# Optimization experiments

Hardware: AMD Instinct MI355X
Metric: run time of the kernel (lower is better)

## Reference

```python
import jax, jax.numpy as jnp
import numpy as np

N, E, NODE_DIM, HID = 10000, 160000, 16, 128
N_CONV = 8  # 4 encoder + 4 decoder EdgeConv layers


def setup_inputs() -> dict:
    key = jax.random.key(0)
    ks = jax.random.split(key, 12)

    def lin(k, fan_in, shape):
        return (jax.random.normal(k, shape, jnp.float32) / np.sqrt(fan_in)).astype(jnp.float32)

    return {
        "x": jax.random.normal(ks[0], (N, NODE_DIM), jnp.float32),
        "edge_index": jax.random.randint(ks[1], (2, E), 0, N, jnp.int32),
        "t": jax.random.uniform(ks[2], (1,), jnp.float32),
        "node_emb_W": lin(ks[3], NODE_DIM, (NODE_DIM, HID)),
        "node_emb_b": jnp.zeros((HID,), jnp.float32),
        "conv_W1": lin(ks[4], 2 * HID, (N_CONV, 2 * HID, HID)),
        "conv_b1": jnp.zeros((N_CONV, HID), jnp.float32),
        "conv_W2": lin(ks[5], HID, (N_CONV, HID, HID)),
        "conv_b2": jnp.zeros((N_CONV, HID), jnp.float32),
        "enc_fc_W": lin(ks[6], HID, (HID, HID)),
        "enc_fc_b": jnp.zeros((HID,), jnp.float32),
        "dec_fc_W": lin(ks[7], HID, (HID, NODE_DIM)),
        "dec_fc_b": jnp.zeros((NODE_DIM,), jnp.float32),
        "time_proj_W": lin(ks[8], 64, (64, NODE_DIM)),
        "time_proj_b": jnp.zeros((NODE_DIM,), jnp.float32),
    }


def _edge_conv(x, src, dst, W1, b1, W2, b2):
    # PyG EdgeConv (aggr='max'): message = mlp(cat[x_i, x_j - x_i]); x_i = x[dst], x_j = x[src]
    xi = x[dst]                      # [E', H]
    xj = x[src]                      # [E', H]
    m = jnp.concatenate([xi, xj - xi], axis=1)           # [E', 2H]
    m = jnp.maximum(m @ W1 + b1, 0.0) @ W2 + b2          # [E', H]
    return jax.ops.segment_max(m, dst, num_segments=x.shape[0])


def reference(x, edge_index, t, node_emb_W, node_emb_b, conv_W1, conv_b1,
              conv_W2, conv_b2, enc_fc_W, enc_fc_b, dec_fc_W, dec_fc_b,
              time_proj_W, time_proj_b):
    n = x.shape[0]
    # add_self_loops (done once; identical across layers)
    loop = jnp.arange(n, dtype=edge_index.dtype)
    src = jnp.concatenate([edge_index[0], loop])
    dst = jnp.concatenate([edge_index[1], loop])

    # sinusoidal time embedding -> projection to node_dim
    freq = jnp.exp(jnp.linspace(-4.0, 4.0, 32).astype(x.dtype))
    t_emb = jnp.concatenate([jnp.sin(t * freq), jnp.cos(t * freq)], axis=-1)  # [64]
    t_emb = t_emb @ time_proj_W + time_proj_b                                  # [node_dim]

    h = x + t_emb[None, :]
    # encoder
    h = h @ node_emb_W + node_emb_b
    for i in range(4):
        h = _edge_conv(h, src, dst, conv_W1[i], conv_b1[i], conv_W2[i], conv_b2[i])
    h = h @ enc_fc_W + enc_fc_b
    # decoder
    for i in range(4, 8):
        h = _edge_conv(h, src, dst, conv_W1[i], conv_b1[i], conv_W2[i], conv_b2[i])
    return h @ dec_fc_W + dec_fc_b
```

## Files before the change

### kernel.cpp

```cpp
#include <hip/hip_runtime.h>
#include <hip/hip_fp16.h>

typedef _Float16 half8 __attribute__((ext_vector_type(8)));
typedef float f32x4 __attribute__((ext_vector_type(4)));
typedef float f32x16 __attribute__((ext_vector_type(16)));

#define HID 128
#define NDIM 16
#define NCONV 8
#define ECAP 64

static __device__ __forceinline__ half8 load_h8(const _Float16* p) {
    return *(const half8*)p;
}

__global__ void prep_weights(const float* __restrict__ W1, const float* __restrict__ W2,
                             const float* __restrict__ dW, const float* __restrict__ b1,
                             const float* __restrict__ eW, const int* __restrict__ ei,
                             _Float16* __restrict__ WABT, _Float16* __restrict__ W2T,
                             _Float16* __restrict__ dWT, float* __restrict__ biasAB,
                             _Float16* __restrict__ eW16,
                             int* __restrict__ cnt, int* __restrict__ eltab, int E) {
    int idx = blockIdx.x * blockDim.x + threadIdx.x;
    int total = NCONV * HID * HID;
    if (idx < total) {
        int l = idx / (HID * HID);
        int r = idx % (HID * HID);
        int k = r / HID;
        int j = r % HID;
        const float* w1 = W1 + (size_t)l * 2 * HID * HID;
        float top = w1[k * HID + j];
        float bot = w1[(HID + k) * HID + j];
        _Float16* wab = WABT + (size_t)l * 2 * HID * HID;
        wab[j * HID + k] = (_Float16)(top - bot);
        wab[(HID + j) * HID + k] = (_Float16)bot;
        const float* w2 = W2 + (size_t)l * HID * HID;
        W2T[(size_t)l * HID * HID + j * HID + k] = (_Float16)w2[k * HID + j];
    } else if (idx < total + 16 * HID) {
        int r = idx - total;
        int j = r / HID;
        int k = r % HID;
        dWT[j * HID + k] = (_Float16)dW[k * NDIM + j];
    } else if (idx < total + 16 * HID + NCONV * 256) {
        int r = idx - total - 16 * HID;
        int l = r >> 8;
        int c = r & 255;
        biasAB[l * 256 + c] = (c < HID) ? b1[l * HID + c] : 0.f;
    } else if (idx < total + 16 * HID + NCONV * 256 + HID * HID) {
        int r = idx - total - 16 * HID - NCONV * 256;
        eW16[r] = (_Float16)eW[r];
    }
    int gsz = gridDim.x * blockDim.x;
    for (int e = idx; e < E; e += gsz) {
        int dv = ei[E + e];
        int pos = atomicAdd(&cnt[dv], 1);
        if (pos < ECAP) eltab[(size_t)dv * ECAP + pos] = ei[e];
    }
}

__global__ __launch_bounds__(512) void node_emb_ab(const float* __restrict__ x,
                                                   const float* __restrict__ t,
                                                   const float* __restrict__ tpW,
                                                   const float* __restrict__ tpb,
                                                   const float* __restrict__ neW,
                                                   const float* __restrict__ neb,
                                                   const _Float16* __restrict__ WABT0,
                                                   const float* __restrict__ biasAB0,
                                                   _Float16* __restrict__ Atab,
                                                   _Float16* __restrict__ Btab,
                                                   const _Float16* __restrict__ eW16,
                                                   const _Float16* __restrict__ WABT4old,
                                                   const float* __restrict__ b1_4,
                                                   const float* __restrict__ eb,
                                                   _Float16* __restrict__ WENC,
                                                   float* __restrict__ biasENC, int n) {
    int bid = blockIdx.x;
    int tid = threadIdx.x;
    int ngroups = (n + 15) >> 4;
    int lane = tid & 63;
    int wv = tid >> 6;
    int c = lane & 15;
    int kq = lane >> 4;

    if (bid >= ngroups) {
        int xb = bid - ngroups;
        if (xb < 16) {
            int gw = xb * 8 + wv;
            int jt = gw >> 3;
            int kt = gw & 7;
            half8 a[4], b[4];
            #pragma unroll
            for (int kb = 0; kb < 4; kb++) {
                a[kb] = load_h8(eW16 + (size_t)(kt * 16 + c) * HID + kb * 32 + kq * 8);
                b[kb] = load_h8(WABT4old + (size_t)(jt * 16 + c) * HID + kb * 32 + kq * 8);
            }
            f32x4 acc = {0.f, 0.f, 0.f, 0.f};
            #pragma unroll
            for (int kb = 0; kb < 4; kb++)
                acc = __builtin_amdgcn_mfma_f32_16x16x32_f16(a[kb], b[kb], acc, 0, 0, 0);
            #pragma unroll
            for (int r = 0; r < 4; r++)
                WENC[(size_t)(jt * 16 + c) * HID + kt * 16 + kq * 4 + r] = (_Float16)acc[r];
        } else if (tid < 256) {
            float acc = (tid < HID) ? b1_4[tid] : 0.f;
            const _Float16* row = WABT4old + (size_t)tid * HID;
            for (int q = 0; q < HID; q++) acc += eb[q] * (float)row[q];
            biasENC[tid] = acc;
        }
        return;
    }

    __shared__ float sc[64];
    __shared__ float temb[NDIM];
    __shared__ _Float16 hlds[16][136];
    float tv = t[0];
    if (tid < 32) {
        float f = expf(-4.0f + 8.0f * (float)tid / 31.0f);
        sc[tid] = sinf(tv * f);
        sc[32 + tid] = cosf(tv * f);
    }
    __syncthreads();
    if (tid < 16) {
        float acc = tpb[tid];
        for (int k = 0; k < 64; k++) acc += sc[k] * tpW[k * NDIM + tid];
        temb[tid] = acc;
    }
    __syncthreads();

    int gbase = bid * 16;
    for (int idx = tid; idx < 16 * HID; idx += 512) {
        int r = idx >> 7;
        int j = idx & 127;
        int v = gbase + r;
        float acc = 0.f;
        if (v < n) {
            const float* xr = x + (size_t)v * NDIM;
            acc = neb[j];
            #pragma unroll
            for (int d = 0; d < NDIM; d++) acc += (xr[d] + temb[d]) * neW[d * HID + j];
        }
        hlds[r][j] = (_Float16)acc;
    }
    __syncthreads();

    half8 a[4];
    #pragma unroll
    for (int kb = 0; kb < 4; kb++)
        a[kb] = load_h8(&hlds[c][kb * 32 + kq * 8]);
    #pragma unroll
    for (int p = 0; p < 2; p++) {
        int jt = wv + p * 8;
        int wrow = jt * 16 + c;
        f32x4 acc = {0.f, 0.f, 0.f, 0.f};
        #pragma unroll
        for (int kb = 0; kb < 4; kb++) {
            half8 b = load_h8(WABT0 + (size_t)wrow * HID + kb * 32 + kq * 8);
            acc = __builtin_amdgcn_mfma_f32_16x16x32_f16(a[kb], b, acc, 0, 0, 0);
        }
        float bv = biasAB0[wrow];
        _Float16* dst = (wrow < HID) ? Atab : Btab;
        int dcol = wrow & (HID - 1);
        #pragma unroll
        for (int r = 0; r < 4; r++) {
            int row = gbase + kq * 4 + r;
            if (row < n) dst[(size_t)row * HID + dcol] = (_Float16)(acc[r] + bv);
        }
    }
}

__global__ __launch_bounds__(512) void fused_conv(const _Float16* __restrict__ Acur,
                                                  const _Float16* __restrict__ Bcur,
                                                  const _Float16* __restrict__ W2T_l,
                                                  const float* __restrict__ b2_l,
                                                  const int* __restrict__ cnt,
                                                  const int* __restrict__ eltab,
                                                  const _Float16* __restrict__ WABT_n,
                                                  const float* __restrict__ biasAB_n,
                                                  _Float16* __restrict__ Anxt,
                                                  _Float16* __restrict__ Bnxt,
                                                  const _Float16* __restrict__ dWT,
                                                  const float* __restrict__ db,
                                                  float* __restrict__ out,
                                                  int last, int n) {
    __shared__ _Float16 w2s[2048 * 8];
    __shared__ float b2s[HID];
    __shared__ _Float16 hlds[16][136];

    int tid = threadIdx.x;
    #pragma unroll
    for (int i = 0; i < 4; i++) {
        int fid = i * 512 + tid;
        int ln = fid & 63;
        int grp = fid >> 6;
        int kb = grp >> 2;
        int cb = grp & 3;
        *(half8*)(w2s + (size_t)fid * 8) =
            load_h8(W2T_l + (size_t)(cb * 32 + (ln & 31)) * HID + kb * 16 + (ln >> 5) * 8);
    }
    if (tid < HID) b2s[tid] = b2_l[tid];
    __syncthreads();

    int lane = tid & 63;
    int wv = tid >> 6;
    int er = lane & 31;
    int hi = lane >> 5;
    int c = lane & 15;
    int kq = lane >> 4;

    int g = blockIdx.x;
    int gbase = g * 16;

    int vA = gbase + wv;
    int vB = gbase + wv + 8;
    int dgA = 0, dgB = 0;
    if (vA < n) { dgA = cnt[vA]; dgA = (dgA > ECAP) ? ECAP : dgA; }
    if (vB < n) { dgB = cnt[vB]; dgB = (dgB > ECAP) ? ECAP : dgB; }
    int srcA = (er < dgA) ? eltab[(size_t)vA * ECAP + er] : vA;
    int srcB = (er < dgB) ? eltab[(size_t)vB * ECAP + er] : vB;

    auto ec_node = [&](int v, int dg, int src0, int row) {
        float macc0 = -3.0e38f, macc1 = -3.0e38f, macc2 = -3.0e38f, macc3 = -3.0e38f;
        if (v < n) {
            int ntile = (dg + 32) >> 5;
            int src = src0;
            for (int tI = 0; tI < ntile; tI++) {
                const _Float16* ap = Acur + (size_t)v * HID + hi * 8;
                const _Float16* bp = Bcur + (size_t)src * HID + hi * 8;
                half8 s[8];
                #pragma unroll
                for (int kb = 0; kb < 8; kb++) {
                    half8 t2 = load_h8(ap + kb * 16) + load_h8(bp + kb * 16);
                    #pragma unroll
                    for (int e2 = 0; e2 < 8; e2++) t2[e2] = (t2[e2] > (_Float16)0) ? t2[e2] : (_Float16)0;
                    s[kb] = t2;
                }
                int en = (tI + 1) * 32 + er;
                int srcn = (tI + 1 < ntile && en < dg) ? eltab[(size_t)v * ECAP + en] : v;

#define CB_BLOCK(CB, MREF)                                                              \
                {                                                                       \
                    f32x16 d;                                                           \
                    _Pragma("unroll")                                                   \
                    for (int e2 = 0; e2 < 16; e2++) d[e2] = 0.f;                        \
                    _Pragma("unroll")                                                   \
                    for (int kb = 0; kb < 8; kb++) {                                    \
                        half8 w = *(const half8*)(w2s + ((size_t)((kb * 4 + CB) * 64 + lane)) * 8); \
                        d = __builtin_amdgcn_mfma_f32_32x32x16_f16(s[kb], w, d, 0, 0, 0); \
                    }                                                                   \
                    float m0 = fmaxf(fmaxf(d[0], d[1]), fmaxf(d[2], d[3]));             \
                    float m1 = fmaxf(fmaxf(d[4], d[5]), fmaxf(d[6], d[7]));             \
                    float m2 = fmaxf(fmaxf(d[8], d[9]), fmaxf(d[10], d[11]));           \
                    float m3 = fmaxf(fmaxf(d[12], d[13]), fmaxf(d[14], d[15]));         \
                    MREF = fmaxf(MREF, fmaxf(fmaxf(m0, m1), fmaxf(m2, m3)));            \
                }
                CB_BLOCK(0, macc0)
                __builtin_amdgcn_sched_barrier(0);
                CB_BLOCK(1, macc1)
                __builtin_amdgcn_sched_barrier(0);
                CB_BLOCK(2, macc2)
                __builtin_amdgcn_sched_barrier(0);
                CB_BLOCK(3, macc3)
#undef CB_BLOCK
                src = srcn;
            }
        }
        float m0 = fmaxf(macc0, __shfl_xor(macc0, 32)) + b2s[er];
        float m1 = fmaxf(macc1, __shfl_xor(macc1, 32)) + b2s[32 + er];
        float m2 = fmaxf(macc2, __shfl_xor(macc2, 32)) + b2s[64 + er];
        float m3 = fmaxf(macc3, __shfl_xor(macc3, 32)) + b2s[96 + er];
        if (lane < 32) {
            hlds[row][er]      = (_Float16)m0;
            hlds[row][32 + er] = (_Float16)m1;
            hlds[row][64 + er] = (_Float16)m2;
            hlds[row][96 + er] = (_Float16)m3;
        }
    };

    ec_node(vA, dgA, srcA, wv);
    ec_node(vB, dgB, srcB, wv + 8);
    __syncthreads();

    if (!last) {
        half8 a[4];
        #pragma unroll
        for (int kb = 0; kb < 4; kb++)
            a[kb] = load_h8(&hlds[c][kb * 32 + kq * 8]);
        #pragma unroll
        for (int p = 0; p < 2; p++) {
            int jt = wv + p * 8;
            int wrow = jt * 16 + c;
            f32x4 acc = {0.f, 0.f, 0.f, 0.f};
            #pragma unroll
            for (int kb = 0; kb < 4; kb++) {
                half8 b = load_h8(WABT_n + (size_t)wrow * HID + kb * 32 + kq * 8);
                acc = __builtin_amdgcn_mfma_f32_16x16x32_f16(a[kb], b, acc, 0, 0, 0);
            }
            float bv = biasAB_n[wrow];
            _Float16* dst = (wrow < HID) ? Anxt : Bnxt;
            int dcol = wrow & (HID - 1);
            #pragma unroll
            for (int r = 0; r < 4; r++) {
                int row = gbase + kq * 4 + r;
                if (row < n) dst[(size_t)row * HID + dcol] = (_Float16)(acc[r] + bv);
            }
        }
    } else if (wv == 0) {
        half8 a[4];
        #pragma unroll
        for (int kb = 0; kb < 4; kb++)
            a[kb] = load_h8(&hlds[c][kb * 32 + kq * 8]);
        f32x4 acc = {0.f, 0.f, 0.f, 0.f};
        #pragma unroll
        for (int kb = 0; kb < 4; kb++) {
            half8 b = load_h8(dWT + (size_t)c * HID + kb * 32 + kq * 8);
            acc = __builtin_amdgcn_mfma_f32_16x16x32_f16(a[kb], b, acc, 0, 0, 0);
        }
        float bv = db[c];
        #pragma unroll
        for (int r = 0; r < 4; r++) {
            int row = gbase + kq * 4 + r;
            if (row < n) out[(size_t)row * NDIM + c] = acc[r] + bv;
        }
    }
}

extern "C" void kernel_launch(void* const* d_in, const int* in_sizes, int n_in,
                              void* d_out, int out_size, void* d_ws, size_t ws_size,
                              hipStream_t stream) {
    const float* x   = (const float*)d_in[0];
    const int*   ei  = (const int*)d_in[1];
    const float* t   = (const float*)d_in[2];
    const float* neW = (const float*)d_in[3];
    const float* neb = (const float*)d_in[4];
    const float* cW1 = (const float*)d_in[5];
    const float* cb1 = (const float*)d_in[6];
    const float* cW2 = (const float*)d_in[7];
    const float* cb2 = (const float*)d_in[8];
    const float* eW  = (const float*)d_in[9];
    const float* eb  = (const float*)d_in[10];
    const float* dW  = (const float*)d_in[11];
    const float* db  = (const float*)d_in[12];
    const float* tpW = (const float*)d_in[13];
    const float* tpb = (const float*)d_in[14];

    int N = in_sizes[0] / NDIM;
    int E = in_sizes[1] / 2;

    char* w = (char*)d_ws;
    auto alloc = [&](size_t bytes) {
        void* p = (void*)w;
        w += (bytes + 255) & ~(size_t)255;
        return p;
    };
    _Float16*  Atab0  = (_Float16*)alloc((size_t)N * HID * 2);
    _Float16*  Btab0  = (_Float16*)alloc((size_t)N * HID * 2);
    _Float16*  Atab1  = (_Float16*)alloc((size_t)N * HID * 2);
    _Float16*  Btab1  = (_Float16*)alloc((size_t)N * HID * 2);
    _Float16*  WABT   = (_Float16*)alloc((size_t)NCONV * 2 * HID * HID * 2);
    _Float16*  W2T    = (_Float16*)alloc((size_t)NCONV * HID * HID * 2);
    _Float16*  dWT    = (_Float16*)alloc((size_t)16 * HID * 2);
    _Float16*  eW16   = (_Float16*)alloc((size_t)HID * HID * 2);
    _Float16*  WENC   = (_Float16*)alloc((size_t)2 * HID * HID * 2);
    float*     biasAB = (float*)alloc((size_t)NCONV * 256 * 4);
    float*     biasENC= (float*)alloc((size_t)256 * 4);
    int*       cnt    = (int*)alloc((size_t)N * 4);
    int*       eltab  = (int*)alloc((size_t)N * ECAP * 4);

    hipMemsetAsync(cnt, 0, (size_t)N * 4, stream);
    int prep_total = NCONV * HID * HID + 16 * HID + NCONV * 256 + HID * HID;
    prep_weights<<<(prep_total + 255) / 256, 256, 0, stream>>>(cW1, cW2, dW, cb1, eW, ei,
                                                               WABT, W2T, dWT, biasAB,
                                                               eW16, cnt, eltab, E);
    int nmt = (N + 15) / 16;
    node_emb_ab<<<nmt + 17, 512, 0, stream>>>(x, t, tpW, tpb, neW, neb,
                                              WABT, biasAB, Atab0, Btab0,
                                              eW16, WABT + (size_t)4 * 2 * HID * HID,
                                              cb1 + (size_t)4 * HID, eb, WENC, biasENC, N);

    for (int l = 0; l < NCONV; l++) {
        const _Float16* Acur = (l & 1) ? Atab1 : Atab0;
        const _Float16* Bcur = (l & 1) ? Btab1 : Btab0;
        _Float16* Anxt = (l & 1) ? Atab0 : Atab1;
        _Float16* Bnxt = (l & 1) ? Btab0 : Btab1;
        int ln = (l + 1 < NCONV) ? (l + 1) : 0;
        const _Float16* wabn = (l == 3) ? WENC : WABT + (size_t)ln * 2 * HID * HID;
        const float*    babn = (l == 3) ? biasENC : biasAB + (size_t)ln * 256;
        fused_conv<<<nmt, 512, 0, stream>>>(Acur, Bcur,
                                            W2T + (size_t)l * HID * HID,
                                            cb2 + (size_t)l * HID,
                                            cnt, eltab,
                                            wabn, babn,
                                            Anxt, Bnxt,
                                            dWT, db, (float*)d_out,
                                            (l == NCONV - 1) ? 1 : 0, N);
    }
}
```

Baseline: 253.8 us.

## Pack two low-degree nodes per MFMA tile and move edge bucketing into embed kernel

When both nodes a wave handles have at most 15 incoming edges (plus self loop), their edges are packed into one 32-row MFMA tile, so the wave runs one set of W2 MFMAs instead of two, each of which was mostly padding. Average degree is about 17 with self loops, so many node pairs qualify. The memset of the degree counters is folded into prep_weights, and the edge bucketing (atomics) moves from prep_weights into node_emb_ab, removing a memset launch. The cost is a divergent code path and more branching per block.

```diff
diff --git a/kernel.cpp b/kernel.cpp
--- a/kernel.cpp
+++ b/kernel.cpp
@@ -16,11 +16,11 @@
 
 __global__ void prep_weights(const float* __restrict__ W1, const float* __restrict__ W2,
                              const float* __restrict__ dW, const float* __restrict__ b1,
-                             const float* __restrict__ eW, const int* __restrict__ ei,
+                             const float* __restrict__ eW,
                              _Float16* __restrict__ WABT, _Float16* __restrict__ W2T,
                              _Float16* __restrict__ dWT, float* __restrict__ biasAB,
                              _Float16* __restrict__ eW16,
-                             int* __restrict__ cnt, int* __restrict__ eltab, int E) {
+                             int* __restrict__ cnt, int n) {
     int idx = blockIdx.x * blockDim.x + threadIdx.x;
     int total = NCONV * HID * HID;
     if (idx < total) {
@@ -49,12 +49,8 @@
     } else if (idx < total + 16 * HID + NCONV * 256 + HID * HID) {
         int r = idx - total - 16 * HID - NCONV * 256;
         eW16[r] = (_Float16)eW[r];
-    }
-    int gsz = gridDim.x * blockDim.x;
-    for (int e = idx; e < E; e += gsz) {
-        int dv = ei[E + e];
-        int pos = atomicAdd(&cnt[dv], 1);
-        if (pos < ECAP) eltab[(size_t)dv * ECAP + pos] = ei[e];
+    } else if (idx < total + 16 * HID + NCONV * 256 + HID * HID + n) {
+        cnt[idx - total - 16 * HID - NCONV * 256 - HID * HID] = 0;
     }
 }
 
@@ -73,9 +69,24 @@
                                                    const float* __restrict__ b1_4,
                                                    const float* __restrict__ eb,
                                                    _Float16* __restrict__ WENC,
-                                                   float* __restrict__ biasENC, int n) {
+                                                   float* __restrict__ biasENC,
+                                                   const int* __restrict__ ei,
+                                                   int* __restrict__ cnt,
+                                                   int* __restrict__ eltab,
+                                                   int n, int E) {
     int bid = blockIdx.x;
     int tid = threadIdx.x;
+
+    {
+        int gtid = bid * 512 + tid;
+        int gsz = gridDim.x * 512;
+        for (int e = gtid; e < E; e += gsz) {
+            int dv = ei[E + e];
+            int pos = atomicAdd(&cnt[dv], 1);
+            if (pos < ECAP) eltab[(size_t)dv * ECAP + pos] = ei[e];
+        }
+    }
+
     int ngroups = (n + 15) >> 4;
     int lane = tid & 63;
     int wv = tid >> 6;
@@ -215,69 +226,119 @@
     int dgA = 0, dgB = 0;
     if (vA < n) { dgA = cnt[vA]; dgA = (dgA > ECAP) ? ECAP : dgA; }
     if (vB < n) { dgB = cnt[vB]; dgB = (dgB > ECAP) ? ECAP : dgB; }
-    int srcA = (er < dgA) ? eltab[(size_t)vA * ECAP + er] : vA;
-    int srcB = (er < dgB) ? eltab[(size_t)vB * ECAP + er] : vB;
-
-    auto ec_node = [&](int v, int dg, int src0, int row) {
-        float macc0 = -3.0e38f, macc1 = -3.0e38f, macc2 = -3.0e38f, macc3 = -3.0e38f;
-        if (v < n) {
-            int ntile = (dg + 32) >> 5;
-            int src = src0;
-            for (int tI = 0; tI < ntile; tI++) {
-                const _Float16* ap = Acur + (size_t)v * HID + hi * 8;
-                const _Float16* bp = Bcur + (size_t)src * HID + hi * 8;
-                half8 s[8];
-                #pragma unroll
-                for (int kb = 0; kb < 8; kb++) {
-                    half8 t2 = load_h8(ap + kb * 16) + load_h8(bp + kb * 16);
+
+    auto write_row = [&](int row, float m0, float m1, float m2, float m3) {
+        float a0 = fmaxf(m0, __shfl_xor(m0, 32)) + b2s[er];
+        float a1 = fmaxf(m1, __shfl_xor(m1, 32)) + b2s[32 + er];
+        float a2 = fmaxf(m2, __shfl_xor(m2, 32)) + b2s[64 + er];
+        float a3 = fmaxf(m3, __shfl_xor(m3, 32)) + b2s[96 + er];
+        if (lane < 32) {
+            hlds[row][er]      = (_Float16)a0;
+            hlds[row][32 + er] = (_Float16)a1;
+            hlds[row][64 + er] = (_Float16)a2;
+            hlds[row][96 + er] = (_Float16)a3;
+        }
+    };
+
+    bool packed = (vB < n) && (dgA <= 15) && (dgB <= 15);
+    if (packed) {
+        int pnode = (er < 16) ? vA : vB;
+        int pe = er & 15;
+        int pdg = (er < 16) ? dgA : dgB;
+        int psrc = (pe < pdg) ? eltab[(size_t)pnode * ECAP + pe] : pnode;
+        const _Float16* ap = Acur + (size_t)pnode * HID + hi * 8;
+        const _Float16* bp = Bcur + (size_t)psrc * HID + hi * 8;
+        half8 s[8];
+        #pragma unroll
+        for (int kb = 0; kb < 8; kb++) {
+            half8 t2 = load_h8(ap + kb * 16) + load_h8(bp + kb * 16);
+            #pragma unroll
+            for (int e2 = 0; e2 < 8; e2++) t2[e2] = (t2[e2] > (_Float16)0) ? t2[e2] : (_Float16)0;
+            s[kb] = t2;
+        }
+        float mA0, mA1, mA2, mA3, mB0, mB1, mB2, mB3;
+#define CBP(CB, MA, MB)                                                                 \
+        {                                                                               \
+            f32x16 d;                                                                   \
+            _Pragma("unroll")                                                           \
+            for (int e2 = 0; e2 < 16; e2++) d[e2] = 0.f;                                \
+            _Pragma("unroll")                                                           \
+            for (int kb = 0; kb < 8; kb++) {                                            \
+                half8 w = *(const half8*)(w2s + ((size_t)((kb * 4 + CB) * 64 + lane)) * 8); \
+                d = __builtin_amdgcn_mfma_f32_32x32x16_f16(s[kb], w, d, 0, 0, 0);       \
+            }                                                                           \
+            float tA = fmaxf(fmaxf(fmaxf(d[0], d[1]), fmaxf(d[2], d[3])),               \
+                             fmaxf(fmaxf(d[4], d[5]), fmaxf(d[6], d[7])));              \
+            float tB = fmaxf(fmaxf(fmaxf(d[8], d[9]), fmaxf(d[10], d[11])),             \
+                             fmaxf(fmaxf(d[12], d[13]), fmaxf(d[14], d[15])));          \
+            MA = tA; MB = tB;                                                           \
+        }
+        CBP(0, mA0, mB0)
+        __builtin_amdgcn_sched_barrier(0);
+        CBP(1, mA1, mB1)
+        __builtin_amdgcn_sched_barrier(0);
+        CBP(2, mA2, mB2)
+        __builtin_amdgcn_sched_barrier(0);
+        CBP(3, mA3, mB3)
+#undef CBP
+        write_row(wv, mA0, mA1, mA2, mA3);
+        write_row(wv + 8, mB0, mB1, mB2, mB3);
+    } else {
+        int srcA = (er < dgA) ? eltab[(size_t)vA * ECAP + er] : vA;
+        int srcB = (er < dgB) ? eltab[(size_t)vB * ECAP + er] : vB;
+
+        auto ec_node = [&](int v, int dg, int src0, int row) {
+            float macc0 = -3.0e38f, macc1 = -3.0e38f, macc2 = -3.0e38f, macc3 = -3.0e38f;
+            if (v < n) {
+                int ntile = (dg + 32) >> 5;
+                int src = src0;
+                for (int tI = 0; tI < ntile; tI++) {
+                    const _Float16* ap = Acur + (size_t)v * HID + hi * 8;
+                    const _Float16* bp = Bcur + (size_t)src * HID + hi * 8;
+                    half8 s[8];
                     #pragma unroll
-                    for (int e2 = 0; e2 < 8; e2++) t2[e2] = (t2[e2] > (_Float16)0) ? t2[e2] : (_Float16)0;
-                    s[kb] = t2;
+                    for (int kb = 0; kb < 8; kb++) {
+                        half8 t2 = load_h8(ap + kb * 16) + load_h8(bp + kb * 16);
+                        #pragma unroll
+                        for (int e2 = 0; e2 < 8; e2++) t2[e2] = (t2[e2] > (_Float16)0) ? t2[e2] : (_Float16)0;
+                        s[kb] = t2;
+                    }
+                    int en = (tI + 1) * 32 + er;
+                    int srcn = (tI + 1 < ntile && en < dg) ? eltab[(size_t)v * ECAP + en] : v;
+
+#define CB_BLOCK(CB, MREF)                                                              \
+                    {                                                                   \
+                        f32x16 d;                                                       \
+                        _Pragma("unroll")                                               \
+                        for (int e2 = 0; e2 < 16; e2++) d[e2] = 0.f;                    \
+                        _Pragma("unroll")                                               \
+                        for (int kb = 0; kb < 8; kb++) {                                \
+                            half8 w = *(const half8*)(w2s + ((size_t)((kb * 4 + CB) * 64 + lane)) * 8); \
+                            d = __builtin_amdgcn_mfma_f32_32x32x16_f16(s[kb], w, d, 0, 0, 0); \
+                        }                                                               \
+                        float m0 = fmaxf(fmaxf(d[0], d[1]), fmaxf(d[2], d[3]));         \
+                        float m1 = fmaxf(fmaxf(d[4], d[5]), fmaxf(d[6], d[7]));         \
+                        float m2 = fmaxf(fmaxf(d[8], d[9]), fmaxf(d[10], d[11]));       \
+                        float m3 = fmaxf(fmaxf(d[12], d[13]), fmaxf(d[14], d[15]));     \
+                        MREF = fmaxf(MREF, fmaxf(fmaxf(m0, m1), fmaxf(m2, m3)));        \
+                    }
+                    CB_BLOCK(0, macc0)
+                    __builtin_amdgcn_sched_barrier(0);
+                    CB_BLOCK(1, macc1)
+                    __builtin_amdgcn_sched_barrier(0);
+                    CB_BLOCK(2, macc2)
+                    __builtin_amdgcn_sched_barrier(0);
+                    CB_BLOCK(3, macc3)
+#undef CB_BLOCK
+                    src = srcn;
                 }
-                int en = (tI + 1) * 32 + er;
-                int srcn = (tI + 1 < ntile && en < dg) ? eltab[(size_t)v * ECAP + en] : v;
-
-#define CB_BLOCK(CB, MREF)                                                              \
-                {                                                                       \
-                    f32x16 d;                                                           \
-                    _Pragma("unroll")                                                   \
-                    for (int e2 = 0; e2 < 16; e2++) d[e2] = 0.f;                        \
-                    _Pragma("unroll")                                                   \
-                    for (int kb = 0; kb < 8; kb++) {                                    \
-                        half8 w = *(const half8*)(w2s + ((size_t)((kb * 4 + CB) * 64 + lane)) * 8); \
-                        d = __builtin_amdgcn_mfma_f32_32x32x16_f16(s[kb], w, d, 0, 0, 0); \
-                    }                                                                   \
-                    float m0 = fmaxf(fmaxf(d[0], d[1]), fmaxf(d[2], d[3]));             \
-                    float m1 = fmaxf(fmaxf(d[4], d[5]), fmaxf(d[6], d[7]));             \
-                    float m2 = fmaxf(fmaxf(d[8], d[9]), fmaxf(d[10], d[11]));           \
-                    float m3 = fmaxf(fmaxf(d[12], d[13]), fmaxf(d[14], d[15]));         \
-                    MREF = fmaxf(MREF, fmaxf(fmaxf(m0, m1), fmaxf(m2, m3)));            \
-                }
-                CB_BLOCK(0, macc0)
-                __builtin_amdgcn_sched_barrier(0);
-                CB_BLOCK(1, macc1)
-                __builtin_amdgcn_sched_barrier(0);
-                CB_BLOCK(2, macc2)
-                __builtin_amdgcn_sched_barrier(0);
-                CB_BLOCK(3, macc3)
-#undef CB_BLOCK
-                src = srcn;
             }
-        }
-        float m0 = fmaxf(macc0, __shfl_xor(macc0, 32)) + b2s[er];
-        float m1 = fmaxf(macc1, __shfl_xor(macc1, 32)) + b2s[32 + er];
-        float m2 = fmaxf(macc2, __shfl_xor(macc2, 32)) + b2s[64 + er];
-        float m3 = fmaxf(macc3, __shfl_xor(macc3, 32)) + b2s[96 + er];
-        if (lane < 32) {
-            hlds[row][er]      = (_Float16)m0;
-            hlds[row][32 + er] = (_Float16)m1;
-            hlds[row][64 + er] = (_Float16)m2;
-            hlds[row][96 + er] = (_Float16)m3;
-        }
-    };
-
-    ec_node(vA, dgA, srcA, wv);
-    ec_node(vB, dgB, srcB, wv + 8);
+            write_row(row, macc0, macc1, macc2, macc3);
+        };
+
+        ec_node(vA, dgA, srcA, wv);
+        ec_node(vB, dgB, srcB, wv + 8);
+    }
     __syncthreads();
 
     if (!last) {
@@ -366,16 +427,16 @@
     int*       cnt    = (int*)alloc((size_t)N * 4);
     int*       eltab  = (int*)alloc((size_t)N * ECAP * 4);
 
-    hipMemsetAsync(cnt, 0, (size_t)N * 4, stream);
-    int prep_total = NCONV * HID * HID + 16 * HID + NCONV * 256 + HID * HID;
-    prep_weights<<<(prep_total + 255) / 256, 256, 0, stream>>>(cW1, cW2, dW, cb1, eW, ei,
+    int prep_total = NCONV * HID * HID + 16 * HID + NCONV * 256 + HID * HID + N;
+    prep_weights<<<(prep_total + 255) / 256, 256, 0, stream>>>(cW1, cW2, dW, cb1, eW,
                                                                WABT, W2T, dWT, biasAB,
-                                                               eW16, cnt, eltab, E);
+                                                               eW16, cnt, N);
     int nmt = (N + 15) / 16;
     node_emb_ab<<<nmt + 17, 512, 0, stream>>>(x, t, tpW, tpb, neW, neb,
                                               WABT, biasAB, Atab0, Btab0,
                                               eW16, WABT + (size_t)4 * 2 * HID * HID,
-                                              cb1 + (size_t)4 * HID, eb, WENC, biasENC, N);
+                                              cb1 + (size_t)4 * HID, eb, WENC, biasENC,
+                                              ei, cnt, eltab, N, E);
 
     for (int l = 0; l < NCONV; l++) {
         const _Float16* Acur = (l & 1) ? Atab1 : Atab0;
```

After: 243.7 us (median of 2 runs). -4.0%, faster.
